# Kernel tuning notes

Hardware: AMD Instinct MI355X
Metric: run time of the kernel (lower is better)

## Reference

```python
import jax, jax.numpy as jnp
import numpy as np

B, N, F_IN, F_OUT = 64, 1024, 256, 64


def setup_inputs() -> dict:
    key = jax.random.key(0)
    k1, k2, k3, k4 = jax.random.split(key, 4)
    # xavier_uniform with gain=1.414 ~= sqrt(2): limit = gain*sqrt(6/(fan_in+fan_out))
    limW = 1.414 * np.sqrt(6.0 / (F_IN + F_OUT))
    lima = 1.414 * np.sqrt(6.0 / (2 * F_OUT + 1))
    return {
        "input": jax.random.normal(k1, (B, N, F_IN), dtype=jnp.float32),
        "adj": jax.random.randint(k2, (B, N, N), 0, 2, dtype=jnp.int32),
        "W": jax.random.uniform(k3, (F_IN, F_OUT), jnp.float32, -limW, limW),
        "a": jax.random.uniform(k4, (2 * F_OUT, 1), jnp.float32, -lima, lima),
    }


def reference(input, adj, W, a):
    # h = input @ W : (B, N, Fo)
    h = jnp.matmul(input, W)
    Bs, n, Fo = h.shape
    a1 = a[:Fo, 0]   # applied to the (scrambled) left block of a_input
    a2 = a[Fo:, 0]   # applied to the tiled right block

    # The original builds a_input by repeat_interleave(N, dim=2).view -> the left
    # block's row (i*N + j) holds h[b, i, (j*Fo + t)//N] for t in [0, Fo).
    # Its dot with a1 is therefore h[b, i, :] @ M[j, :] with
    #   M[j, f] = sum_{t : (j*Fo+t)//N == f} a1[t]
    idx = (jnp.arange(n)[:, None] * Fo + jnp.arange(Fo)[None, :]) // n  # (N, Fo), values in [0, Fo)
    rows = jnp.broadcast_to(jnp.arange(n)[:, None], (n, Fo))
    M = jnp.zeros((n, Fo), h.dtype).at[rows, idx].add(jnp.broadcast_to(a1, (n, Fo)))  # (N, Fo)

    e1 = jnp.einsum("bif,jf->bij", h, M)          # left-block contribution, (B, N, N)
    e2 = jnp.einsum("bjf,f->bj", h, a2)           # right block = h tiled over i, (B, N)
    # leakyrelu result is immediately overwritten by relu in the source; only relu matters
    e = jax.nn.relu(e1 + e2[:, None, :])

    neg = jnp.asarray(-9e15, e.dtype)
    attention = jax.nn.softmax(jnp.where(adj > 0, e, neg), axis=2)
    # F.dropout omitted (inference / deterministic reference)
    h_prime = jnp.matmul(attention, h)            # (B, N, Fo)
    return jax.nn.elu(h_prime)                    # concat=True branch
```

## Files before the change

kernel.cpp:

```cpp
#include <hip/hip_runtime.h>
#include <math.h>

#define B_   64
#define N_   1024
#define FIN_ 256
#define FO_  64

typedef __attribute__((ext_vector_type(4))) float f32x4;
typedef __attribute__((ext_vector_type(8))) short short8;

__device__ __forceinline__ unsigned fbits(float f){ union{float f;unsigned u;}v; v.f=f; return v.u; }
__device__ __forceinline__ float bcast(unsigned u){ union{unsigned u;float f;}v; v.u=u; return v.f; }
__device__ __forceinline__ float bf2f(unsigned short h){ return bcast(((unsigned)h)<<16); }
__device__ __forceinline__ float hi_part(float x){ return bcast(fbits(x) & 0xffff0000u); }
__device__ __forceinline__ unsigned pack_hi(float x0, float x1){
    return (fbits(x1) & 0xffff0000u) | (fbits(x0) >> 16);
}

union U8 { unsigned u[4]; short8 s8; };

__global__ void k0_wt(const float* __restrict__ W,
                      unsigned short* __restrict__ WThi,
                      unsigned short* __restrict__ WTlo)
{
    const int idx = blockIdx.x * 256 + threadIdx.x;
    const int k = idx >> 6, f = idx & 63;
    const float w = W[idx];
    const float hf = hi_part(w);
    WThi[f * FIN_ + k] = (unsigned short)(fbits(w) >> 16);
    WTlo[f * FIN_ + k] = (unsigned short)(fbits(w - hf) >> 16);
}

__global__ __launch_bounds__(256, 4) void k1_hproj(
    const float* __restrict__ input,
    const unsigned short* __restrict__ WThi,
    const unsigned short* __restrict__ WTlo,
    const float* __restrict__ a,
    unsigned short* __restrict__ hbT,
    unsigned short* __restrict__ hrT,
    float* __restrict__ e2)
{
    __shared__ unsigned short eb[64 * 72];
    __shared__ unsigned short er[64 * 72];

    const int t  = threadIdx.x;
    const int lm = t & 15, lk = (t >> 4) & 3, wm0 = (t >> 6) * 16;
    const int r0 = blockIdx.x * 64;
    const int b  = blockIdx.x >> 4;
    const int jb = r0 & (N_ - 1);

    const float* arow = input + (size_t)(r0 + wm0 + lm) * FIN_;

    f32x4 acc[4] = {};
    float4 xa = *reinterpret_cast<const float4*>(&arow[lk * 8]);
    float4 xb = *reinterpret_cast<const float4*>(&arow[lk * 8 + 4]);

    #pragma unroll
    for (int ks = 0; ks < 8; ++ks) {
        const float x[8] = { xa.x, xa.y, xa.z, xa.w, xb.x, xb.y, xb.z, xb.w };
        U8 ah, al;
        #pragma unroll
        for (int p = 0; p < 4; ++p) {
            const float f0 = x[2 * p], f1 = x[2 * p + 1];
            ah.u[p] = pack_hi(f0, f1);
            al.u[p] = pack_hi(f0 - hi_part(f0), f1 - hi_part(f1));
        }
        if (ks < 7) {
            xa = *reinterpret_cast<const float4*>(&arow[(ks + 1) * 32 + lk * 8]);
            xb = *reinterpret_cast<const float4*>(&arow[(ks + 1) * 32 + lk * 8 + 4]);
        }
        #pragma unroll
        for (int nt = 0; nt < 4; ++nt) {
            const int off = (nt * 16 + lm) * FIN_ + ks * 32 + lk * 8;
            const short8 bh = *reinterpret_cast<const short8*>(&WThi[off]);
            const short8 bl = *reinterpret_cast<const short8*>(&WTlo[off]);
            acc[nt] = __builtin_amdgcn_mfma_f32_16x16x32_bf16(ah.s8, bh, acc[nt], 0, 0, 0);
            acc[nt] = __builtin_amdgcn_mfma_f32_16x16x32_bf16(ah.s8, bl, acc[nt], 0, 0, 0);
            acc[nt] = __builtin_amdgcn_mfma_f32_16x16x32_bf16(al.s8, bh, acc[nt], 0, 0, 0);
        }
    }

    float ap[4];
    #pragma unroll
    for (int nt = 0; nt < 4; ++nt) ap[nt] = a[FO_ + nt * 16 + lm];

    #pragma unroll
    for (int reg = 0; reg < 4; ++reg) {
        const int row = wm0 + lk * 4 + reg;
        float e2p = 0.f;
        #pragma unroll
        for (int nt = 0; nt < 4; ++nt) {
            const float hv = acc[nt][reg];
            e2p += hv * ap[nt];
            const float hf = hi_part(hv);
            const int f = nt * 16 + lm;
            eb[f * 72 + row] = (unsigned short)(fbits(hv) >> 16);
            er[f * 72 + row] = (unsigned short)(fbits(hv - hf) >> 16);
        }
        e2p += __shfl_xor(e2p, 1);
        e2p += __shfl_xor(e2p, 2);
        e2p += __shfl_xor(e2p, 4);
        e2p += __shfl_xor(e2p, 8);
        if (lm == 0) e2[r0 + row] = e2p;
    }
    __syncthreads();

    {
        const int f = t >> 2, seg = t & 3;
        const size_t gb = ((size_t)(b * FO_ + f)) * N_ + jb + seg * 16;
        *reinterpret_cast<short8*>(&hbT[gb]) =
            *reinterpret_cast<const short8*>(&eb[f * 72 + seg * 16]);
        *reinterpret_cast<short8*>(&hbT[gb + 8]) =
            *reinterpret_cast<const short8*>(&eb[f * 72 + seg * 16 + 8]);
        *reinterpret_cast<short8*>(&hrT[gb]) =
            *reinterpret_cast<const short8*>(&er[f * 72 + seg * 16]);
        *reinterpret_cast<short8*>(&hrT[gb + 8]) =
            *reinterpret_cast<const short8*>(&er[f * 72 + seg * 16 + 8]);
    }
}

__global__ __launch_bounds__(256, 4) void k2_attn(
    const unsigned short* __restrict__ hbT,
    const unsigned short* __restrict__ hrT,
    const int*   __restrict__ adj,
    const float* __restrict__ a,
    const float* __restrict__ e2,
    float* __restrict__ out)
{
    const int t  = threadIdx.x;
    const int lm = t & 15, lk = (t >> 4) & 3, wm0 = (t >> 6) * 16;
    const int b  = blockIdx.y;
    const int i0 = blockIdx.x * 64;
    const int irow = i0 + wm0 + lm;

    const int*   adjrow = adj + ((size_t)b * N_ + irow) * N_;
    const float* e2b    = e2 + (size_t)b * N_;
    const unsigned short* hbTb = hbT + (size_t)b * FO_ * N_;
    const unsigned short* hrTb = hrT + (size_t)b * FO_ * N_;

    float S1 = 0.f;
    #pragma unroll
    for (int f = 0; f < FO_; f += 4) {
        const float4 av = *reinterpret_cast<const float4*>(&a[f]);
        S1 += av.x + av.y + av.z + av.w;
    }

    f32x4 acc[4] = {};
    float den = 0.f;

    int4 aC0 = *reinterpret_cast<const int4*>(&adjrow[lk * 8]);
    int4 aC1 = *reinterpret_cast<const int4*>(&adjrow[lk * 8 + 4]);

    #pragma unroll 1
    for (int tile = 0; tile < 32; ++tile) {
        const int jt = tile * 32;
        int4 aN0, aN1;
        if (tile < 31) {
            aN0 = *reinterpret_cast<const int4*>(&adjrow[jt + 32 + lk * 8]);
            aN1 = *reinterpret_cast<const int4*>(&adjrow[jt + 32 + lk * 8 + 4]);
        }
        const float4 ea = *reinterpret_cast<const float4*>(&e2b[jt + lk * 8]);
        const float4 eb2 = *reinterpret_cast<const float4*>(&e2b[jt + lk * 8 + 4]);
        const int g = (jt >> 4) + (lk >> 1);
        const float c2 = bf2f(hbTb[(size_t)g * N_ + irow]) +
                         bf2f(hrTb[(size_t)g * N_ + irow]);
        const float cg = S1 * c2;

        const int   aa[8] = { aC0.x, aC0.y, aC0.z, aC0.w, aC1.x, aC1.y, aC1.z, aC1.w };
        const float ee[8] = { ea.x, ea.y, ea.z, ea.w, eb2.x, eb2.y, eb2.z, eb2.w };
        float hf[8], lf[8];
        #pragma unroll
        for (int d = 0; d < 8; ++d) {
            const float ev = fmaxf(cg + ee[d], 0.f);
            const float w  = aa[d] ? __expf(ev) : 0.f;
            hf[d] = hi_part(w);
            lf[d] = w - hf[d];
            den += hf[d] + hi_part(lf[d]);
        }
        U8 whi, wlo;
        #pragma unroll
        for (int p = 0; p < 4; ++p) {
            whi.u[p] = pack_hi(hf[2 * p], hf[2 * p + 1]);
            wlo.u[p] = pack_hi(lf[2 * p], lf[2 * p + 1]);
        }

        #pragma unroll
        for (int nt = 0; nt < 4; ++nt) {
            const size_t off = (size_t)(nt * 16 + lm) * N_ + jt + lk * 8;
            const short8 bh = *reinterpret_cast<const short8*>(&hbTb[off]);
            const short8 br = *reinterpret_cast<const short8*>(&hrTb[off]);
            acc[nt] = __builtin_amdgcn_mfma_f32_16x16x32_bf16(whi.s8, bh, acc[nt], 0, 0, 0);
            acc[nt] = __builtin_amdgcn_mfma_f32_16x16x32_bf16(whi.s8, br, acc[nt], 0, 0, 0);
            acc[nt] = __builtin_amdgcn_mfma_f32_16x16x32_bf16(wlo.s8, bh, acc[nt], 0, 0, 0);
        }
        aC0 = aN0; aC1 = aN1;
    }

    den += __shfl_xor(den, 16);
    den += __shfl_xor(den, 32);

    #pragma unroll
    for (int reg = 0; reg < 4; ++reg) {
        const int m = lk * 4 + reg;
        const float dm = __shfl(den, m);
        const float inv = 1.0f / dm;
        #pragma unroll
        for (int nt = 0; nt < 4; ++nt) {
            const float x = acc[nt][reg] * inv;
            const float y = (x > 0.f) ? x : expm1f(x);
            out[((size_t)b * N_ + i0 + wm0 + m) * FO_ + nt * 16 + lm] = y;
        }
    }
}

extern "C" void kernel_launch(void* const* d_in, const int* in_sizes, int n_in,
                              void* d_out, int out_size, void* d_ws, size_t ws_size,
                              hipStream_t stream) {
    const float* input = (const float*)d_in[0];
    const int*   adj   = (const int*)d_in[1];
    const float* W     = (const float*)d_in[2];
    const float* a     = (const float*)d_in[3];
    float* out = (float*)d_out;

    char* ws = (char*)d_ws;
    unsigned short* hbT  = (unsigned short*)(ws);
    unsigned short* hrT  = (unsigned short*)(ws + (8u << 20));
    float*          e2   = (float*)(ws + (16u << 20));
    unsigned short* WThi = (unsigned short*)(ws + (16u << 20) + (256u << 10));
    unsigned short* WTlo = WThi + FO_ * FIN_;

    k0_wt   <<<dim3(64),              dim3(256), 0, stream>>>(W, WThi, WTlo);
    k1_hproj<<<dim3((B_ * N_) / 64),  dim3(256), 0, stream>>>(input, WThi, WTlo, a, hbT, hrT, e2);
    k2_attn <<<dim3(N_ / 64, B_),     dim3(256), 0, stream>>>(hbT, hrT, adj, a, e2, out);
}
```

Before: 533.6 us.

## Restructure attention kernel with LDS double-buffering, factored exp, MFMA denominator

The projection kernel now computes the transposed product (W as the A operand, input as B), writes h hi/lo and a precomputed fp32 c1 = S1*h directly, and reduces e2 through shared memory. The attention kernel stages h and the attention weights in swizzled, double-buffered LDS and prefetches two tiles ahead. It rewrites exp(relu(c+e2)) as exp(c)*exp(e2) with exp(e2) precomputed per block, which removes most per-element exp calls. The softmax denominator is now computed with an MFMA against a ones vector, and blocks are remapped across XCDs. The costs are an extra fp32 c1T buffer written and read, extra LDS traffic and barriers, and a possible accuracy change from the factored exp.

```diff
diff --git a/kernel.cpp b/kernel.cpp
--- a/kernel.cpp
+++ b/kernel.cpp
@@ -11,204 +11,264 @@
 
 __device__ __forceinline__ unsigned fbits(float f){ union{float f;unsigned u;}v; v.f=f; return v.u; }
 __device__ __forceinline__ float bcast(unsigned u){ union{unsigned u;float f;}v; v.u=u; return v.f; }
-__device__ __forceinline__ float bf2f(unsigned short h){ return bcast(((unsigned)h)<<16); }
 __device__ __forceinline__ float hi_part(float x){ return bcast(fbits(x) & 0xffff0000u); }
 __device__ __forceinline__ unsigned pack_hi(float x0, float x1){
     return (fbits(x1) & 0xffff0000u) | (fbits(x0) >> 16);
 }
-
 union U8 { unsigned u[4]; short8 s8; };
 
 __global__ void k0_wt(const float* __restrict__ W,
-                      unsigned short* __restrict__ WThi,
-                      unsigned short* __restrict__ WTlo)
+                      unsigned short* __restrict__ WTfhi,
+                      unsigned short* __restrict__ WTflo)
 {
-    const int idx = blockIdx.x * 256 + threadIdx.x;
-    const int k = idx >> 6, f = idx & 63;
-    const float w = W[idx];
-    const float hf = hi_part(w);
-    WThi[f * FIN_ + k] = (unsigned short)(fbits(w) >> 16);
-    WTlo[f * FIN_ + k] = (unsigned short)(fbits(w - hf) >> 16);
+    const int tid = blockIdx.x * 256 + threadIdx.x;
+    const int k = tid >> 6, f = tid & 63;
+    const float wv = W[tid];
+    const int idx = ((((k >> 5) * 4 + ((k >> 3) & 3)) * 64 + f) << 3) + (k & 7);
+    WTfhi[idx] = (unsigned short)(fbits(wv) >> 16);
+    WTflo[idx] = (unsigned short)(fbits(wv - hi_part(wv)) >> 16);
 }
 
 __global__ __launch_bounds__(256, 4) void k1_hproj(
     const float* __restrict__ input,
-    const unsigned short* __restrict__ WThi,
-    const unsigned short* __restrict__ WTlo,
+    const unsigned short* __restrict__ WTfhi,
+    const unsigned short* __restrict__ WTflo,
     const float* __restrict__ a,
     unsigned short* __restrict__ hbT,
     unsigned short* __restrict__ hrT,
+    float* __restrict__ c1T,
     float* __restrict__ e2)
 {
-    __shared__ unsigned short eb[64 * 72];
-    __shared__ unsigned short er[64 * 72];
-
-    const int t  = threadIdx.x;
-    const int lm = t & 15, lk = (t >> 4) & 3, wm0 = (t >> 6) * 16;
+    __shared__ float e2L[4][64];
+    const int t = threadIdx.x;
+    const int l = t & 63, lm = l & 15, lk = l >> 4, w = t >> 6;
     const int r0 = blockIdx.x * 64;
-    const int b  = blockIdx.x >> 4;
-    const int jb = r0 & (N_ - 1);
-
-    const float* arow = input + (size_t)(r0 + wm0 + lm) * FIN_;
+    const int b = r0 >> 10, jb = r0 & (N_ - 1);
+
+    float S1 = 0.f;
+    #pragma unroll
+    for (int f = 0; f < FO_; f += 4) {
+        const float4 av = *reinterpret_cast<const float4*>(&a[f]);
+        S1 += av.x + av.y + av.z + av.w;
+    }
 
     f32x4 acc[4] = {};
-    float4 xa = *reinterpret_cast<const float4*>(&arow[lk * 8]);
-    float4 xb = *reinterpret_cast<const float4*>(&arow[lk * 8 + 4]);
-
+    float4 cur[8], nxt[8];
+    const float* bbase = input + (size_t)r0 * FIN_;
+
+    auto loadB = [&](float4* dst, int ks) {
+        #pragma unroll
+        for (int nt = 0; nt < 4; ++nt) {
+            const float* p = bbase + (size_t)(nt * 16 + lm) * FIN_ + ks * 32 + lk * 8;
+            dst[nt * 2]     = *reinterpret_cast<const float4*>(p);
+            dst[nt * 2 + 1] = *reinterpret_cast<const float4*>(p + 4);
+        }
+    };
+
+    loadB(cur, 0);
     #pragma unroll
     for (int ks = 0; ks < 8; ++ks) {
-        const float x[8] = { xa.x, xa.y, xa.z, xa.w, xb.x, xb.y, xb.z, xb.w };
-        U8 ah, al;
-        #pragma unroll
-        for (int p = 0; p < 4; ++p) {
-            const float f0 = x[2 * p], f1 = x[2 * p + 1];
-            ah.u[p] = pack_hi(f0, f1);
-            al.u[p] = pack_hi(f0 - hi_part(f0), f1 - hi_part(f1));
+        if (ks < 7) loadB(nxt, ks + 1);
+        const int abase = (((ks * 4 + lk) * 64) + w * 16 + lm) * 8;
+        const short8 ahi = *reinterpret_cast<const short8*>(&WTfhi[abase]);
+        const short8 alo = *reinterpret_cast<const short8*>(&WTflo[abase]);
+        #pragma unroll
+        for (int nt = 0; nt < 4; ++nt) {
+            const float4 x0 = cur[nt * 2], x1 = cur[nt * 2 + 1];
+            const float xs[8] = { x0.x, x0.y, x0.z, x0.w, x1.x, x1.y, x1.z, x1.w };
+            U8 bh, bl;
+            #pragma unroll
+            for (int p = 0; p < 4; ++p) {
+                const float f0 = xs[2 * p], f1 = xs[2 * p + 1];
+                bh.u[p] = pack_hi(f0, f1);
+                bl.u[p] = pack_hi(f0 - hi_part(f0), f1 - hi_part(f1));
+            }
+            acc[nt] = __builtin_amdgcn_mfma_f32_16x16x32_bf16(ahi, bh.s8, acc[nt], 0, 0, 0);
+            acc[nt] = __builtin_amdgcn_mfma_f32_16x16x32_bf16(ahi, bl.s8, acc[nt], 0, 0, 0);
+            acc[nt] = __builtin_amdgcn_mfma_f32_16x16x32_bf16(alo, bh.s8, acc[nt], 0, 0, 0);
         }
         if (ks < 7) {
-            xa = *reinterpret_cast<const float4*>(&arow[(ks + 1) * 32 + lk * 8]);
-            xb = *reinterpret_cast<const float4*>(&arow[(ks + 1) * 32 + lk * 8 + 4]);
-        }
-        #pragma unroll
-        for (int nt = 0; nt < 4; ++nt) {
-            const int off = (nt * 16 + lm) * FIN_ + ks * 32 + lk * 8;
-            const short8 bh = *reinterpret_cast<const short8*>(&WThi[off]);
-            const short8 bl = *reinterpret_cast<const short8*>(&WTlo[off]);
-            acc[nt] = __builtin_amdgcn_mfma_f32_16x16x32_bf16(ah.s8, bh, acc[nt], 0, 0, 0);
-            acc[nt] = __builtin_amdgcn_mfma_f32_16x16x32_bf16(ah.s8, bl, acc[nt], 0, 0, 0);
-            acc[nt] = __builtin_amdgcn_mfma_f32_16x16x32_bf16(al.s8, bh, acc[nt], 0, 0, 0);
-        }
-    }
-
-    float ap[4];
-    #pragma unroll
-    for (int nt = 0; nt < 4; ++nt) ap[nt] = a[FO_ + nt * 16 + lm];
-
+            #pragma unroll
+            for (int q = 0; q < 8; ++q) cur[q] = nxt[q];
+        }
+    }
+
+    float a2v[4];
+    #pragma unroll
+    for (int reg = 0; reg < 4; ++reg) a2v[reg] = a[FO_ + w * 16 + lk * 4 + reg];
+
+    float ep[4] = { 0.f, 0.f, 0.f, 0.f };
     #pragma unroll
     for (int reg = 0; reg < 4; ++reg) {
-        const int row = wm0 + lk * 4 + reg;
-        float e2p = 0.f;
+        const int f = w * 16 + lk * 4 + reg;
         #pragma unroll
         for (int nt = 0; nt < 4; ++nt) {
             const float hv = acc[nt][reg];
-            e2p += hv * ap[nt];
-            const float hf = hi_part(hv);
-            const int f = nt * 16 + lm;
-            eb[f * 72 + row] = (unsigned short)(fbits(hv) >> 16);
-            er[f * 72 + row] = (unsigned short)(fbits(hv - hf) >> 16);
-        }
-        e2p += __shfl_xor(e2p, 1);
-        e2p += __shfl_xor(e2p, 2);
-        e2p += __shfl_xor(e2p, 4);
-        e2p += __shfl_xor(e2p, 8);
-        if (lm == 0) e2[r0 + row] = e2p;
+            const size_t o = (size_t)(b * FO_ + f) * N_ + jb + nt * 16 + lm;
+            hbT[o] = (unsigned short)(fbits(hv) >> 16);
+            hrT[o] = (unsigned short)(fbits(hv - hi_part(hv)) >> 16);
+            c1T[o] = S1 * hv;
+            ep[nt] += hv * a2v[reg];
+        }
+    }
+    #pragma unroll
+    for (int nt = 0; nt < 4; ++nt) {
+        ep[nt] += __shfl_xor(ep[nt], 16);
+        ep[nt] += __shfl_xor(ep[nt], 32);
+    }
+    if (lk == 0) {
+        #pragma unroll
+        for (int nt = 0; nt < 4; ++nt) e2L[w][nt * 16 + lm] = ep[nt];
     }
     __syncthreads();
-
-    {
-        const int f = t >> 2, seg = t & 3;
-        const size_t gb = ((size_t)(b * FO_ + f)) * N_ + jb + seg * 16;
-        *reinterpret_cast<short8*>(&hbT[gb]) =
-            *reinterpret_cast<const short8*>(&eb[f * 72 + seg * 16]);
-        *reinterpret_cast<short8*>(&hbT[gb + 8]) =
-            *reinterpret_cast<const short8*>(&eb[f * 72 + seg * 16 + 8]);
-        *reinterpret_cast<short8*>(&hrT[gb]) =
-            *reinterpret_cast<const short8*>(&er[f * 72 + seg * 16]);
-        *reinterpret_cast<short8*>(&hrT[gb + 8]) =
-            *reinterpret_cast<const short8*>(&er[f * 72 + seg * 16 + 8]);
-    }
+    if (t < 64) e2[r0 + t] = e2L[0][t] + e2L[1][t] + e2L[2][t] + e2L[3][t];
 }
 
 __global__ __launch_bounds__(256, 4) void k2_attn(
     const unsigned short* __restrict__ hbT,
     const unsigned short* __restrict__ hrT,
+    const float* __restrict__ c1T,
     const int*   __restrict__ adj,
-    const float* __restrict__ a,
     const float* __restrict__ e2,
     float* __restrict__ out)
 {
-    const int t  = threadIdx.x;
-    const int lm = t & 15, lk = (t >> 4) & 3, wm0 = (t >> 6) * 16;
-    const int b  = blockIdx.y;
-    const int i0 = blockIdx.x * 64;
-    const int irow = i0 + wm0 + lm;
-
-    const int*   adjrow = adj + ((size_t)b * N_ + irow) * N_;
-    const float* e2b    = e2 + (size_t)b * N_;
+    __shared__ unsigned short hlds[2][64 * 64];
+    __shared__ unsigned short wlds[2][64 * 64];
+    __shared__ float e2lds[N_];
+    __shared__ float E2lds[N_];
+
+    const int t = threadIdx.x;
+    const int l = t & 63, lm = l & 15, lk = l >> 4, w = t >> 6;
+    const int wm0 = w * 16;
+
+    const int raw = blockIdx.x;
+    const int wg  = (raw & 7) * 128 + (raw >> 3);
+    const int b   = wg >> 4;
+    const int i0  = (wg & 15) * 64;
+
+    const int la = l & 7, r8 = l >> 3;
+    const int row0 = wm0 + r8, row1 = wm0 + 8 + r8;
+    const int gl = la >> 2;
+    const int fs = wm0 + (l >> 2), sj = l & 3;
+
+    const size_t badj = (size_t)b * N_ * N_;
+    const int* adjr0 = adj + badj + (size_t)(i0 + row0) * N_ + la * 4;
+    const int* adjr1 = adj + badj + (size_t)(i0 + row1) * N_ + la * 4;
     const unsigned short* hbTb = hbT + (size_t)b * FO_ * N_;
     const unsigned short* hrTb = hrT + (size_t)b * FO_ * N_;
-
-    float S1 = 0.f;
-    #pragma unroll
-    for (int f = 0; f < FO_; f += 4) {
-        const float4 av = *reinterpret_cast<const float4*>(&a[f]);
-        S1 += av.x + av.y + av.z + av.w;
-    }
+    const float* c1Tb = c1T + (size_t)b * FO_ * N_;
+    const float* e2b  = e2  + (size_t)b * N_;
+    float* outb = out + (size_t)b * N_ * FO_;
 
     f32x4 acc[4] = {};
-    float den = 0.f;
-
-    int4 aC0 = *reinterpret_cast<const int4*>(&adjrow[lk * 8]);
-    int4 aC1 = *reinterpret_cast<const int4*>(&adjrow[lk * 8 + 4]);
+    f32x4 accd = {};
+
+    int4 areg0, areg1;
+    short8 hbreg, hrreg;
+    float c1r0, c1r1;
+
+    auto prefetch = [&](int tile) {
+        const int jt = tile * 32;
+        areg0 = *reinterpret_cast<const int4*>(adjr0 + jt);
+        areg1 = *reinterpret_cast<const int4*>(adjr1 + jt);
+        hbreg = *reinterpret_cast<const short8*>(&hbTb[(size_t)fs * N_ + jt + sj * 8]);
+        hrreg = *reinterpret_cast<const short8*>(&hrTb[(size_t)fs * N_ + jt + sj * 8]);
+        const int g = (jt >> 4) + gl;
+        c1r0 = c1Tb[(size_t)g * N_ + i0 + row0];
+        c1r1 = c1Tb[(size_t)g * N_ + i0 + row1];
+    };
+
+    auto phaseW = [&](int tt, int n) {
+        const int jt = tt * 32;
+        const int swh = (fs & 7) << 3;
+        const int hb0 = fs * 64 + sj * 8;
+        *reinterpret_cast<short8*>(&hlds[n][hb0 ^ swh]) = hbreg;
+        *reinterpret_cast<short8*>(&hlds[n][(hb0 + 32) ^ swh]) = hrreg;
+
+        const float4 e2q = *reinterpret_cast<const float4*>(&e2lds[jt + la * 4]);
+        const float4 E2q = *reinterpret_cast<const float4*>(&E2lds[jt + la * 4]);
+        const float eq[4] = { e2q.x, e2q.y, e2q.z, e2q.w };
+        const float Eq[4] = { E2q.x, E2q.y, E2q.z, E2q.w };
+        #pragma unroll
+        for (int i8 = 0; i8 < 2; ++i8) {
+            const float c = i8 ? c1r1 : c1r0;
+            const int4 av = i8 ? areg1 : areg0;
+            const float ec = __expf(c);
+            const int aa[4] = { av.x, av.y, av.z, av.w };
+            float hfv[4], lfv[4];
+            #pragma unroll
+            for (int d = 0; d < 4; ++d) {
+                const float m  = (c + eq[d] > 0.f) ? ec * Eq[d] : 1.0f;
+                const float wv = aa[d] ? m : 0.0f;
+                hfv[d] = hi_part(wv);
+                lfv[d] = wv - hfv[d];
+            }
+            uint2 whi, wlo;
+            whi.x = pack_hi(hfv[0], hfv[1]); whi.y = pack_hi(hfv[2], hfv[3]);
+            wlo.x = pack_hi(lfv[0], lfv[1]); wlo.y = pack_hi(lfv[2], lfv[3]);
+            const int row = i8 ? row1 : row0;
+            const int sww = (row & 7) << 3;
+            const int wb  = row * 64 + la * 4;
+            *reinterpret_cast<uint2*>(&wlds[n][wb ^ sww]) = whi;
+            *reinterpret_cast<uint2*>(&wlds[n][(wb + 32) ^ sww]) = wlo;
+        }
+    };
+
+    short8 ones;
+    #pragma unroll
+    for (int q = 0; q < 8; ++q) ones[q] = (short)0x3F80;
+
+    auto phaseG = [&](int cb) {
+        const int arow = wm0 + lm;
+        const int swa = (arow & 7) << 3;
+        const int ab  = arow * 64 + lk * 8;
+        const short8 awh = *reinterpret_cast<const short8*>(&wlds[cb][ab ^ swa]);
+        const short8 awl = *reinterpret_cast<const short8*>(&wlds[cb][(ab + 32) ^ swa]);
+        accd = __builtin_amdgcn_mfma_f32_16x16x32_bf16(awh, ones, accd, 0, 0, 0);
+        accd = __builtin_amdgcn_mfma_f32_16x16x32_bf16(awl, ones, accd, 0, 0, 0);
+        #pragma unroll
+        for (int nt = 0; nt < 4; ++nt) {
+            const int f = nt * 16 + lm;
+            const int swb = (f & 7) << 3;
+            const int bb  = f * 64 + lk * 8;
+            const short8 bh = *reinterpret_cast<const short8*>(&hlds[cb][bb ^ swb]);
+            const short8 br = *reinterpret_cast<const short8*>(&hlds[cb][(bb + 32) ^ swb]);
+            acc[nt] = __builtin_amdgcn_mfma_f32_16x16x32_bf16(awh, bh, acc[nt], 0, 0, 0);
+            acc[nt] = __builtin_amdgcn_mfma_f32_16x16x32_bf16(awh, br, acc[nt], 0, 0, 0);
+            acc[nt] = __builtin_amdgcn_mfma_f32_16x16x32_bf16(awl, bh, acc[nt], 0, 0, 0);
+        }
+    };
+
+    {
+        const float4 ev = *reinterpret_cast<const float4*>(&e2b[t * 4]);
+        *reinterpret_cast<float4*>(&e2lds[t * 4]) = ev;
+        float4 Ev;
+        Ev.x = __expf(ev.x); Ev.y = __expf(ev.y);
+        Ev.z = __expf(ev.z); Ev.w = __expf(ev.w);
+        *reinterpret_cast<float4*>(&E2lds[t * 4]) = Ev;
+    }
+    prefetch(0);
+    __syncthreads();
+    phaseW(0, 0);
+    prefetch(1);
+    __syncthreads();
 
     #pragma unroll 1
     for (int tile = 0; tile < 32; ++tile) {
-        const int jt = tile * 32;
-        int4 aN0, aN1;
-        if (tile < 31) {
-            aN0 = *reinterpret_cast<const int4*>(&adjrow[jt + 32 + lk * 8]);
-            aN1 = *reinterpret_cast<const int4*>(&adjrow[jt + 32 + lk * 8 + 4]);
-        }
-        const float4 ea = *reinterpret_cast<const float4*>(&e2b[jt + lk * 8]);
-        const float4 eb2 = *reinterpret_cast<const float4*>(&e2b[jt + lk * 8 + 4]);
-        const int g = (jt >> 4) + (lk >> 1);
-        const float c2 = bf2f(hbTb[(size_t)g * N_ + irow]) +
-                         bf2f(hrTb[(size_t)g * N_ + irow]);
-        const float cg = S1 * c2;
-
-        const int   aa[8] = { aC0.x, aC0.y, aC0.z, aC0.w, aC1.x, aC1.y, aC1.z, aC1.w };
-        const float ee[8] = { ea.x, ea.y, ea.z, ea.w, eb2.x, eb2.y, eb2.z, eb2.w };
-        float hf[8], lf[8];
-        #pragma unroll
-        for (int d = 0; d < 8; ++d) {
-            const float ev = fmaxf(cg + ee[d], 0.f);
-            const float w  = aa[d] ? __expf(ev) : 0.f;
-            hf[d] = hi_part(w);
-            lf[d] = w - hf[d];
-            den += hf[d] + hi_part(lf[d]);
-        }
-        U8 whi, wlo;
-        #pragma unroll
-        for (int p = 0; p < 4; ++p) {
-            whi.u[p] = pack_hi(hf[2 * p], hf[2 * p + 1]);
-            wlo.u[p] = pack_hi(lf[2 * p], lf[2 * p + 1]);
-        }
-
-        #pragma unroll
-        for (int nt = 0; nt < 4; ++nt) {
-            const size_t off = (size_t)(nt * 16 + lm) * N_ + jt + lk * 8;
-            const short8 bh = *reinterpret_cast<const short8*>(&hbTb[off]);
-            const short8 br = *reinterpret_cast<const short8*>(&hrTb[off]);
-            acc[nt] = __builtin_amdgcn_mfma_f32_16x16x32_bf16(whi.s8, bh, acc[nt], 0, 0, 0);
-            acc[nt] = __builtin_amdgcn_mfma_f32_16x16x32_bf16(whi.s8, br, acc[nt], 0, 0, 0);
-            acc[nt] = __builtin_amdgcn_mfma_f32_16x16x32_bf16(wlo.s8, bh, acc[nt], 0, 0, 0);
-        }
-        aC0 = aN0; aC1 = aN1;
-    }
-
-    den += __shfl_xor(den, 16);
-    den += __shfl_xor(den, 32);
+        if (tile < 31) phaseW(tile + 1, (tile + 1) & 1);
+        if (tile < 30) prefetch(tile + 2);
+        phaseG(tile & 1);
+        __syncthreads();
+    }
 
     #pragma unroll
     for (int reg = 0; reg < 4; ++reg) {
-        const int m = lk * 4 + reg;
-        const float dm = __shfl(den, m);
-        const float inv = 1.0f / dm;
+        const int i = i0 + wm0 + lk * 4 + reg;
+        const float inv = 1.0f / accd[reg];
         #pragma unroll
         for (int nt = 0; nt < 4; ++nt) {
             const float x = acc[nt][reg] * inv;
-            const float y = (x > 0.f) ? x : expm1f(x);
-            out[((size_t)b * N_ + i0 + wm0 + m) * FO_ + nt * 16 + lm] = y;
+            outb[(size_t)i * FO_ + nt * 16 + lm] = (x > 0.f) ? x : expm1f(x);
         }
     }
 }
@@ -223,13 +283,15 @@
     float* out = (float*)d_out;
 
     char* ws = (char*)d_ws;
-    unsigned short* hbT  = (unsigned short*)(ws);
-    unsigned short* hrT  = (unsigned short*)(ws + (8u << 20));
-    float*          e2   = (float*)(ws + (16u << 20));
-    unsigned short* WThi = (unsigned short*)(ws + (16u << 20) + (256u << 10));
-    unsigned short* WTlo = WThi + FO_ * FIN_;
-
-    k0_wt   <<<dim3(64),              dim3(256), 0, stream>>>(W, WThi, WTlo);
-    k1_hproj<<<dim3((B_ * N_) / 64),  dim3(256), 0, stream>>>(input, WThi, WTlo, a, hbT, hrT, e2);
-    k2_attn <<<dim3(N_ / 64, B_),     dim3(256), 0, stream>>>(hbT, hrT, adj, a, e2, out);
-}
+    unsigned short* hbT   = (unsigned short*)(ws);
+    unsigned short* hrT   = (unsigned short*)(ws + (8u  << 20));
+    float*          c1T   = (float*)(ws + (16u << 20));
+    float*          e2    = (float*)(ws + (32u << 20));
+    unsigned short* WTfhi = (unsigned short*)(ws + (32u << 20) + (256u << 10));
+    unsigned short* WTflo = WTfhi + FIN_ * FO_;
+
+    k0_wt   <<<dim3(64),             dim3(256), 0, stream>>>(W, WTfhi, WTflo);
+    k1_hproj<<<dim3((B_ * N_) / 64), dim3(256), 0, stream>>>(input, WTfhi, WTflo, a,
+                                                             hbT, hrT, c1T, e2);
+    k2_attn <<<dim3(1024),           dim3(256), 0, stream>>>(hbT, hrT, c1T, adj, e2, out);
+}
```

After: 447.4 us. 1.19x faster.
